# Kernel optimization log

Hardware: AMD Instinct MI355X
Metric: run time of the kernel (lower is better)

The kernel has to match this reference:

```python
import jax, jax.numpy as jnp
import numpy as np

B, N, C, H, D = 4, 2048, 1024, 16, 64
EPS = 1e-6

def setup_inputs() -> dict:
    key = jax.random.key(0)
    k1, k2, k3 = jax.random.split(key, 3)
    hidden_states = jax.random.normal(k1, (B, N, C), dtype=jnp.float32)
    qkv_w = jax.random.normal(k2, (3 * C, C), dtype=jnp.float32) * (C ** -0.5)
    out_w = jax.random.normal(k3, (C, C), dtype=jnp.float32) * (C ** -0.5)
    norm_q_w = jnp.ones((D,), dtype=jnp.float32)
    norm_k_w = jnp.ones((D,), dtype=jnp.float32)
    # RoPE tables: standard theta=10000 frequencies, rotate-half convention
    inv_freq = 1.0 / (10000.0 ** (jnp.arange(0, D, 2, dtype=jnp.float32) / D))
    pos = jnp.arange(N, dtype=jnp.float32)
    angles = pos[:, None] * inv_freq[None, :]              # [N, D/2]
    angles = jnp.concatenate([angles, angles], axis=-1)    # [N, D]
    cos = jnp.cos(angles)
    sin = jnp.sin(angles)
    return {"hidden_states": hidden_states, "cos": cos, "sin": sin,
            "qkv_w": qkv_w, "out_w": out_w,
            "norm_q_w": norm_q_w, "norm_k_w": norm_k_w}

def _rms_norm(x, w):
    # RMSNorm over last dim (head_dim)
    var = jnp.mean(jnp.square(x), axis=-1, keepdims=True)
    return x * jax.lax.rsqrt(var + EPS) * w

def _rotate_half(x):
    x1, x2 = jnp.split(x, 2, axis=-1)
    return jnp.concatenate([-x2, x1], axis=-1)

def reference(hidden_states, cos, sin, qkv_w, out_w, norm_q_w, norm_k_w):
    # fused QKV projection: [B,N,C] -> [B,N,3,H,D]
    qkv = jnp.einsum('bnc,oc->bno', hidden_states, qkv_w).reshape(B, N, 3, H, D)
    q, k, v = qkv[:, :, 0], qkv[:, :, 1], qkv[:, :, 2]   # each [B,N,H,D]
    q = _rms_norm(q, norm_q_w)
    k = _rms_norm(k, norm_k_w)
    # RoPE, broadcast cos/sin [N,D] -> [1,N,1,D]
    c = cos[None, :, None, :]
    s = sin[None, :, None, :]
    q = q * c + _rotate_half(q) * s
    k = k * c + _rotate_half(k) * s
    # SDPA: softmax(q k^T / sqrt(D)) v, no mask
    scale = D ** -0.5
    scores = jnp.einsum('bqhd,bkhd->bhqk', q, k) * scale   # [B,H,N,N]
    probs = jax.nn.softmax(scores, axis=-1)
    attn = jnp.einsum('bhqk,bkhd->bqhd', probs, v).reshape(B, N, C)
    return jnp.einsum('bnc,oc->bno', attn, out_w)
```

## Files before the change

### kernel.cpp

```cpp
#include <hip/hip_runtime.h>
#include <hip/hip_bf16.h>
#include <math.h>

typedef short bf16x8 __attribute__((ext_vector_type(8)));
typedef float f32x4 __attribute__((ext_vector_type(4)));
typedef float f32x16 __attribute__((ext_vector_type(16)));
typedef __hip_bfloat16 bf16;
typedef unsigned int uint;

static constexpr int Bn = 4, Nn = 2048, Cn = 1024, Hn = 16, Dn = 64;
static constexpr float kEps = 1e-6f;
static constexpr float kQScale = 0.125f * 1.44269504088896340f;

#define GLOAD_LDS16(gp, lp)                                                        \
  __builtin_amdgcn_global_load_lds(                                                \
      (const __attribute__((address_space(1))) unsigned int*)(gp),                 \
      (__attribute__((address_space(3))) unsigned int*)(lp), 16, 0, 0)

__device__ __forceinline__ float exp2_fast(float x) {
#if __has_builtin(__builtin_amdgcn_exp2f)
  return __builtin_amdgcn_exp2f(x);
#else
  return exp2f(x);
#endif
}

__global__ __launch_bounds__(256) void cvt_kernel(const float* __restrict__ in,
                                                  bf16* __restrict__ out, int n4) {
  int i = blockIdx.x * 256 + threadIdx.x;
  if (i >= n4) return;
  const float4 v = reinterpret_cast<const float4*>(in)[i];
  bf16 t[4];
  t[0] = __float2bfloat16(v.x); t[1] = __float2bfloat16(v.y);
  t[2] = __float2bfloat16(v.z); t[3] = __float2bfloat16(v.w);
  reinterpret_cast<uint2*>(out)[i] = *reinterpret_cast<const uint2*>(t);
}

template <int EPI>
__global__ __launch_bounds__(256) void gemm_bt(
    const bf16* __restrict__ A, const bf16* __restrict__ Bw,
    float* __restrict__ Cf, bf16* __restrict__ q_raw, bf16* __restrict__ k_raw,
    bf16* __restrict__ v_buf, const float* __restrict__ cosb,
    const float* __restrict__ sinb, const float* __restrict__ nqw,
    const float* __restrict__ nkw, int nxt, int nyt, int N, int K) {
  __shared__ __align__(16) bf16 As[128 * 64];
  __shared__ __align__(16) bf16 Bs[128 * 64];
  const int tid = threadIdx.x;
  const int lane = tid & 63, w = tid >> 6;
  const int wr = w >> 1, wc = w & 1;
  const int l15 = lane & 15, l4 = lane >> 4;
  const int bid = blockIdx.x;
  const int xcd = bid & 7;
  const int kk2 = bid >> 3;
  const int nslab = nxt >> 3;
  const int mtile = kk2 / nslab;
  const int ntile = xcd * nslab + (kk2 % nslab);
  const int m0 = mtile * 128, n0 = ntile * 128;
  f32x4 acc[4][4] = {};

  const int sr = tid >> 3, sc = (tid & 7) * 8;
  const bf16* const Ap = A + (size_t)(m0 + sr) * K + sc;
  const bf16* const Bp = Bw + (size_t)(n0 + sr) * K + sc;
  char* const asd = (char*)As + tid * 16;
  char* const bsd = (char*)Bs + tid * 16;

  for (int k0 = 0; k0 < K; k0 += 64) {
    __syncthreads();
#pragma unroll
    for (int c = 0; c < 4; ++c) {
      GLOAD_LDS16(Ap + (size_t)(c * 32) * K + k0, asd + c * 4096);
      GLOAD_LDS16(Bp + (size_t)(c * 32) * K + k0, bsd + c * 4096);
    }
    __syncthreads();
#pragma unroll
    for (int kc = 0; kc < 2; ++kc) {
      bf16x8 af[4], bfr[4];
#pragma unroll
      for (int mi = 0; mi < 4; ++mi)
        af[mi] = *reinterpret_cast<const bf16x8*>(
            (const char*)As + (wr * 64 + mi * 16 + l15) * 128 + kc * 64 + l4 * 16);
#pragma unroll
      for (int ni = 0; ni < 4; ++ni)
        bfr[ni] = *reinterpret_cast<const bf16x8*>(
            (const char*)Bs + (wc * 64 + ni * 16 + l15) * 128 + kc * 64 + l4 * 16);
#pragma unroll
      for (int mi = 0; mi < 4; ++mi)
#pragma unroll
        for (int ni = 0; ni < 4; ++ni)
          acc[mi][ni] =
              __builtin_amdgcn_mfma_f32_16x16x32_bf16(af[mi], bfr[ni], acc[mi][ni], 0, 0, 0);
    }
  }

  if (EPI == 1) {
#pragma unroll
    for (int mi = 0; mi < 4; ++mi)
#pragma unroll
      for (int ni = 0; ni < 4; ++ni)
#pragma unroll
        for (int r = 0; r < 4; ++r) {
          const int row = m0 + wr * 64 + mi * 16 + l4 * 4 + r;
          const int col = n0 + wc * 64 + ni * 16 + l15;
          Cf[(size_t)row * N + col] = acc[mi][ni][r];
        }
    return;
  }

  const int colbase = n0 + wc * 64;
  const int which = colbase >> 10;
  const int hh = (colbase >> 6) & 15;
  if (which == 2) {
#pragma unroll
    for (int mi = 0; mi < 4; ++mi)
#pragma unroll
      for (int r = 0; r < 4; ++r) {
        const int row = m0 + wr * 64 + mi * 16 + l4 * 4 + r;
        const int b = row >> 11, n = row & (Nn - 1);
#pragma unroll
        for (int ni = 0; ni < 4; ++ni) {
          const int d = ni * 16 + l15;
          const size_t idx = (((size_t)b * Hn + hh) * Nn + n) * Dn + d;
          v_buf[idx] = __float2bfloat16(acc[mi][ni][r]);
        }
      }
    return;
  }
  const float* const wgt = which ? nkw : nqw;
  bf16* const dst = which ? k_raw : q_raw;
  float wv4[4];
#pragma unroll
  for (int ni = 0; ni < 4; ++ni) wv4[ni] = wgt[ni * 16 + l15];
#pragma unroll
  for (int mi = 0; mi < 4; ++mi)
#pragma unroll
    for (int r = 0; r < 4; ++r) {
      const int row = m0 + wr * 64 + mi * 16 + l4 * 4 + r;
      const int b = row >> 11, n = row & (Nn - 1);
      float x0 = acc[mi][0][r], x1 = acc[mi][1][r], x2 = acc[mi][2][r], x3 = acc[mi][3][r];
      float ss = x0 * x0 + x1 * x1 + x2 * x2 + x3 * x3;
      ss += __shfl_xor(ss, 1);
      ss += __shfl_xor(ss, 2);
      ss += __shfl_xor(ss, 4);
      ss += __shfl_xor(ss, 8);
      const float rinv = rsqrtf(ss * (1.f / Dn) + kEps);
      float nx[4] = {x0 * rinv * wv4[0], x1 * rinv * wv4[1], x2 * rinv * wv4[2],
                     x3 * rinv * wv4[3]};
#pragma unroll
      for (int ni = 0; ni < 4; ++ni) {
        const int d = ni * 16 + l15;
        const float c = cosb[n * Dn + d], s = sinb[n * Dn + d];
        const float sgn = (ni < 2) ? -1.f : 1.f;
        float val = nx[ni] * c + sgn * nx[ni ^ 2] * s;
        if (which == 0) val *= kQScale;
        const size_t idx = (((size_t)b * Hn + hh) * Nn + n) * Dn + d;
        dst[idx] = __float2bfloat16(val);
      }
    }
}

__global__ __launch_bounds__(256, 4) void flash_attn(
    const bf16* __restrict__ Qb, const bf16* __restrict__ Kb,
    const bf16* __restrict__ Vb, bf16* __restrict__ Ob) {
  __shared__ __align__(16) char KsB[2][32 * 128];
  __shared__ __align__(16) char VtB[2][64 * 64];
  const int bid = blockIdx.x;
  const int xcd = bid & 7;
  const int kidx = bid >> 3;
  const int bh = xcd * 8 + (kidx >> 4);
  const int q0 = (kidx & 15) * 128;
  const int tid = threadIdx.x, lane = tid & 63, w = tid >> 6;
  const int l31 = lane & 31, hi = lane >> 5;
  const bf16* Qp = Qb + (size_t)bh * Nn * Dn;
  const bf16* Kp = Kb + (size_t)bh * Nn * Dn;
  const bf16* Vp = Vb + (size_t)bh * Nn * Dn;

  const int qrow = q0 + w * 32 + l31;
  bf16x8 qf[4];
#pragma unroll
  for (int dm = 0; dm < 4; ++dm)
    qf[dm] = *reinterpret_cast<const bf16x8*>(&Qp[(size_t)qrow * Dn + dm * 16 + hi * 8]);

  f32x16 Ot0 = {}, Ot1 = {};
  float l_r = 0.f;

  const int skk = tid >> 3, sd0 = (tid & 7) * 8;
  const int srcKe = (((sd0 * 2) ^ ((skk & 7) << 4)) >> 1);

  auto stage_v = [&](char* Vn, const uint4& a) {
    const uint wa[4] = {a.x, a.y, a.z, a.w};
#pragma unroll
    for (int j = 0; j < 8; ++j) {
      const int d = sd0 + j;
      const int xs = (((d >> 1) ^ (d >> 3)) & 3) << 4;
      const unsigned short va = (j & 1) ? (unsigned short)(wa[j >> 1] >> 16)
                                        : (unsigned short)(wa[j >> 1] & 0xffff);
      *reinterpret_cast<unsigned short*>(Vn + d * 64 + ((skk * 2) ^ xs)) = va;
    }
  };

  GLOAD_LDS16(Kp + (size_t)skk * Dn + srcKe, KsB[0] + tid * 16);
  {
    uint4 cv = *reinterpret_cast<const uint4*>(&Vp[(size_t)skk * Dn + sd0]);
    stage_v(VtB[0], cv);
  }
  uint4 nv = *reinterpret_cast<const uint4*>(&Vp[(size_t)(32 + skk) * Dn + sd0]);
  __syncthreads();

  const int swzk_rd = (l31 & 7) << 4;
  const int xs0 = ((((l31) >> 1) ^ ((l31) >> 3)) & 3) << 4;
  const int xs1 = ((((32 + l31) >> 1) ^ ((32 + l31) >> 3)) & 3) << 4;
  int cur = 0;
  for (int k0 = 0; k0 < Nn; k0 += 32) {
    const char* Kc = KsB[cur];
    const char* Vc = VtB[cur];

    if (k0 + 32 < Nn) {
      GLOAD_LDS16(Kp + (size_t)(k0 + 32 + skk) * Dn + srcKe, KsB[cur ^ 1] + tid * 16);
      stage_v(VtB[cur ^ 1], nv);
      if (k0 + 64 < Nn)
        nv = *reinterpret_cast<const uint4*>(&Vp[(size_t)(k0 + 64 + skk) * Dn + sd0]);
    }

    f32x16 S0 = {};
    __builtin_amdgcn_s_setprio(1);
#pragma unroll
    for (int dm = 0; dm < 4; ++dm) {
      bf16x8 kf = *reinterpret_cast<const bf16x8*>(
          Kc + l31 * 128 + ((dm * 32 + hi * 16) ^ swzk_rd));
      S0 = __builtin_amdgcn_mfma_f32_32x32x16_bf16(kf, qf[dm], S0, 0, 0, 0);
    }
    __builtin_amdgcn_s_setprio(0);

#pragma unroll
    for (int i = 0; i < 16; ++i) S0[i] = exp2_fast(S0[i]);
    float ps = 0.f;
    uint wv[8];
#pragma unroll
    for (int c = 0; c < 2; ++c) {
      ps += ((S0[8 * c + 0] + S0[8 * c + 1]) + (S0[8 * c + 2] + S0[8 * c + 3])) +
            ((S0[8 * c + 4] + S0[8 * c + 5]) + (S0[8 * c + 6] + S0[8 * c + 7]));
      uint w0, w1, w2, w3;
      asm("v_cvt_pk_bf16_f32 %0, %1, %2" : "=v"(w0) : "v"(S0[8 * c + 0]), "v"(S0[8 * c + 1]));
      asm("v_cvt_pk_bf16_f32 %0, %1, %2" : "=v"(w1) : "v"(S0[8 * c + 2]), "v"(S0[8 * c + 3]));
      asm("v_cvt_pk_bf16_f32 %0, %1, %2" : "=v"(w2) : "v"(S0[8 * c + 4]), "v"(S0[8 * c + 5]));
      asm("v_cvt_pk_bf16_f32 %0, %1, %2" : "=v"(w3) : "v"(S0[8 * c + 6]), "v"(S0[8 * c + 7]));
      asm("v_permlane32_swap_b32 %0, %1" : "+v"(w0), "+v"(w2));
      asm("v_permlane32_swap_b32 %0, %1" : "+v"(w1), "+v"(w3));
      wv[c * 4 + 0] = w0; wv[c * 4 + 1] = w1;
      wv[c * 4 + 2] = w2; wv[c * 4 + 3] = w3;
    }
    ps += __shfl_xor(ps, 32);
    l_r += ps;

    __builtin_amdgcn_s_setprio(1);
#pragma unroll
    for (int s = 0; s < 2; ++s) {
      const uint4 uu = {wv[s * 4 + 0], wv[s * 4 + 1], wv[s * 4 + 2], wv[s * 4 + 3]};
      const bf16x8 pa = __builtin_bit_cast(bf16x8, uu);
      bf16x8 vf0 = *reinterpret_cast<const bf16x8*>(
          Vc + l31 * 64 + ((s * 32 + hi * 16) ^ xs0));
      Ot0 = __builtin_amdgcn_mfma_f32_32x32x16_bf16(vf0, pa, Ot0, 0, 0, 0);
      bf16x8 vf1 = *reinterpret_cast<const bf16x8*>(
          Vc + (32 + l31) * 64 + ((s * 32 + hi * 16) ^ xs1));
      Ot1 = __builtin_amdgcn_mfma_f32_32x32x16_bf16(vf1, pa, Ot1, 0, 0, 0);
    }
    __builtin_amdgcn_s_setprio(0);

    __syncthreads();
    cur ^= 1;
  }

  const float inv = 1.f / l_r;
  const int b = bh >> 4, h = bh & 15;
#pragma unroll
  for (int dc = 0; dc < 2; ++dc)
#pragma unroll
    for (int a2 = 0; a2 < 4; ++a2) {
      const f32x16& O = dc ? Ot1 : Ot0;
      unsigned short u0 = __bfloat16_as_ushort(__float2bfloat16(O[a2 * 4 + 0] * inv));
      unsigned short u1 = __bfloat16_as_ushort(__float2bfloat16(O[a2 * 4 + 1] * inv));
      unsigned short u2 = __bfloat16_as_ushort(__float2bfloat16(O[a2 * 4 + 2] * inv));
      unsigned short u3 = __bfloat16_as_ushort(__float2bfloat16(O[a2 * 4 + 3] * inv));
      uint2 pk;
      pk.x = (uint)u0 | ((uint)u1 << 16);
      pk.y = (uint)u2 | ((uint)u3 << 16);
      const int col = h * 64 + dc * 32 + a2 * 8 + hi * 4;
      *reinterpret_cast<uint2*>(&Ob[((size_t)(b * Nn + qrow)) * Cn + col]) = pk;
    }
}

extern "C" void kernel_launch(void* const* d_in, const int* in_sizes, int n_in,
                              void* d_out, int out_size, void* d_ws, size_t ws_size,
                              hipStream_t stream) {
  const float* hs   = (const float*)d_in[0];
  const float* cosb = (const float*)d_in[1];
  const float* sinb = (const float*)d_in[2];
  const float* qkvw = (const float*)d_in[3];
  const float* outw = (const float*)d_in[4];
  const float* nqw  = (const float*)d_in[5];
  const float* nkw  = (const float*)d_in[6];
  float* out = (float*)d_out;

  char* ws = (char*)d_ws;
  size_t off = 0;
  bf16* hs_b   = (bf16*)(ws + off); off += (size_t)Bn * Nn * Cn * 2;
  bf16* qkvw_b = (bf16*)(ws + off); off += (size_t)3 * Cn * Cn * 2;
  bf16* outw_b = (bf16*)(ws + off); off += (size_t)Cn * Cn * 2;
  bf16* q_raw  = (bf16*)(ws + off); off += (size_t)Bn * Hn * Nn * Dn * 2;
  bf16* k_raw  = (bf16*)(ws + off); off += (size_t)Bn * Hn * Nn * Dn * 2;
  bf16* v_buf  = (bf16*)(ws + off); off += (size_t)Bn * Hn * Nn * Dn * 2;
  bf16* attn   = (bf16*)(ws + off); off += (size_t)Bn * Nn * Cn * 2;

  cvt_kernel<<<(Bn * Nn * Cn / 4 + 255) / 256, 256, 0, stream>>>(hs, hs_b, Bn * Nn * Cn / 4);
  cvt_kernel<<<(3 * Cn * Cn / 4 + 255) / 256, 256, 0, stream>>>(qkvw, qkvw_b, 3 * Cn * Cn / 4);
  cvt_kernel<<<(Cn * Cn / 4 + 255) / 256, 256, 0, stream>>>(outw, outw_b, Cn * Cn / 4);

  gemm_bt<0><<<24 * 64, 256, 0, stream>>>(
      hs_b, qkvw_b, nullptr, q_raw, k_raw, v_buf, cosb, sinb, nqw, nkw,
      24, 64, 3 * Cn, Cn);

  flash_attn<<<Nn / 128 * Bn * Hn, 256, 0, stream>>>(q_raw, k_raw, v_buf, attn);

  gemm_bt<1><<<8 * 64, 256, 0, stream>>>(
      attn, outw_b, out, nullptr, nullptr, nullptr, nullptr, nullptr, nullptr, nullptr,
      8, 64, Cn, Cn);
}
```

Measured before the change: 223.8 us.

## Double-buffer GEMM LDS tiles and defer softmax row-sum reduction in attention

The projection GEMM now keeps two LDS buffers for A and B, so the global-to-LDS loads for the next K tile are issued before the MFMA work on the current tile. This replaces the two barriers per iteration with one. Separately, the attention kernel accumulates exp values per element into a 16-wide vector and reduces across lanes only once after the loop, removing the per-iteration sum and cross-lane shuffle. The cost is double the GEMM LDS footprint (64 KB per block), which may reduce occupancy, and 16 extra accumulator registers in attention.

```diff
diff --git a/kernel.cpp b/kernel.cpp
--- a/kernel.cpp
+++ b/kernel.cpp
@@ -43,8 +43,8 @@
     bf16* __restrict__ v_buf, const float* __restrict__ cosb,
     const float* __restrict__ sinb, const float* __restrict__ nqw,
     const float* __restrict__ nkw, int nxt, int nyt, int N, int K) {
-  __shared__ __align__(16) bf16 As[128 * 64];
-  __shared__ __align__(16) bf16 Bs[128 * 64];
+  __shared__ __align__(16) bf16 As[2][128 * 64];
+  __shared__ __align__(16) bf16 Bs[2][128 * 64];
   const int tid = threadIdx.x;
   const int lane = tid & 63, w = tid >> 6;
   const int wr = w >> 1, wc = w & 1;
@@ -61,28 +61,38 @@
   const int sr = tid >> 3, sc = (tid & 7) * 8;
   const bf16* const Ap = A + (size_t)(m0 + sr) * K + sc;
   const bf16* const Bp = Bw + (size_t)(n0 + sr) * K + sc;
-  char* const asd = (char*)As + tid * 16;
-  char* const bsd = (char*)Bs + tid * 16;
-
+
+#pragma unroll
+  for (int c = 0; c < 4; ++c) {
+    GLOAD_LDS16(Ap + (size_t)(c * 32) * K, (char*)As[0] + tid * 16 + c * 4096);
+    GLOAD_LDS16(Bp + (size_t)(c * 32) * K, (char*)Bs[0] + tid * 16 + c * 4096);
+  }
+  __syncthreads();
+
+  int cur = 0;
   for (int k0 = 0; k0 < K; k0 += 64) {
-    __syncthreads();
-#pragma unroll
-    for (int c = 0; c < 4; ++c) {
-      GLOAD_LDS16(Ap + (size_t)(c * 32) * K + k0, asd + c * 4096);
-      GLOAD_LDS16(Bp + (size_t)(c * 32) * K + k0, bsd + c * 4096);
-    }
-    __syncthreads();
+    if (k0 + 64 < K) {
+#pragma unroll
+      for (int c = 0; c < 4; ++c) {
+        GLOAD_LDS16(Ap + (size_t)(c * 32) * K + k0 + 64,
+                    (char*)As[cur ^ 1] + tid * 16 + c * 4096);
+        GLOAD_LDS16(Bp + (size_t)(c * 32) * K + k0 + 64,
+                    (char*)Bs[cur ^ 1] + tid * 16 + c * 4096);
+      }
+    }
+    const char* Ac = (const char*)As[cur];
+    const char* Bc = (const char*)Bs[cur];
 #pragma unroll
     for (int kc = 0; kc < 2; ++kc) {
       bf16x8 af[4], bfr[4];
 #pragma unroll
       for (int mi = 0; mi < 4; ++mi)
         af[mi] = *reinterpret_cast<const bf16x8*>(
-            (const char*)As + (wr * 64 + mi * 16 + l15) * 128 + kc * 64 + l4 * 16);
+            Ac + (wr * 64 + mi * 16 + l15) * 128 + kc * 64 + l4 * 16);
 #pragma unroll
       for (int ni = 0; ni < 4; ++ni)
         bfr[ni] = *reinterpret_cast<const bf16x8*>(
-            (const char*)Bs + (wc * 64 + ni * 16 + l15) * 128 + kc * 64 + l4 * 16);
+            Bc + (wc * 64 + ni * 16 + l15) * 128 + kc * 64 + l4 * 16);
 #pragma unroll
       for (int mi = 0; mi < 4; ++mi)
 #pragma unroll
@@ -90,6 +100,8 @@
           acc[mi][ni] =
               __builtin_amdgcn_mfma_f32_16x16x32_bf16(af[mi], bfr[ni], acc[mi][ni], 0, 0, 0);
     }
+    __syncthreads();
+    cur ^= 1;
   }
 
   if (EPI == 1) {
@@ -180,8 +192,7 @@
   for (int dm = 0; dm < 4; ++dm)
     qf[dm] = *reinterpret_cast<const bf16x8*>(&Qp[(size_t)qrow * Dn + dm * 16 + hi * 8]);
 
-  f32x16 Ot0 = {}, Ot1 = {};
-  float l_r = 0.f;
+  f32x16 Ot0 = {}, Ot1 = {}, Lacc = {};
 
   const int skk = tid >> 3, sd0 = (tid & 7) * 8;
   const int srcKe = (((sd0 * 2) ^ ((skk & 7) << 4)) >> 1);
@@ -233,12 +244,11 @@
 
 #pragma unroll
     for (int i = 0; i < 16; ++i) S0[i] = exp2_fast(S0[i]);
-    float ps = 0.f;
+#pragma unroll
+    for (int i = 0; i < 16; ++i) Lacc[i] += S0[i];
     uint wv[8];
 #pragma unroll
     for (int c = 0; c < 2; ++c) {
-      ps += ((S0[8 * c + 0] + S0[8 * c + 1]) + (S0[8 * c + 2] + S0[8 * c + 3])) +
-            ((S0[8 * c + 4] + S0[8 * c + 5]) + (S0[8 * c + 6] + S0[8 * c + 7]));
       uint w0, w1, w2, w3;
       asm("v_cvt_pk_bf16_f32 %0, %1, %2" : "=v"(w0) : "v"(S0[8 * c + 0]), "v"(S0[8 * c + 1]));
       asm("v_cvt_pk_bf16_f32 %0, %1, %2" : "=v"(w1) : "v"(S0[8 * c + 2]), "v"(S0[8 * c + 3]));
@@ -249,8 +259,6 @@
       wv[c * 4 + 0] = w0; wv[c * 4 + 1] = w1;
       wv[c * 4 + 2] = w2; wv[c * 4 + 3] = w3;
     }
-    ps += __shfl_xor(ps, 32);
-    l_r += ps;
 
     __builtin_amdgcn_s_setprio(1);
 #pragma unroll
@@ -269,6 +277,12 @@
     __syncthreads();
     cur ^= 1;
   }
+
+  float l_r = ((Lacc[0] + Lacc[1]) + (Lacc[2] + Lacc[3])) +
+              ((Lacc[4] + Lacc[5]) + (Lacc[6] + Lacc[7])) +
+              ((Lacc[8] + Lacc[9]) + (Lacc[10] + Lacc[11])) +
+              ((Lacc[12] + Lacc[13]) + (Lacc[14] + Lacc[15]));
+  l_r += __shfl_xor(l_r, 32);
 
   const float inv = 1.f / l_r;
   const int b = bh >> 4, h = bh & 15;
```

After: 221.9 us. About the same (-0.9%).
